# Kernel optimization log

Hardware: AMD Instinct MI355X
Metric: run time of the kernel (lower is better)

## Reference

```python
import jax, jax.numpy as jnp
import numpy as np

NUM_USERS = 50000
NUM_ITEMS = 50000
N_NODES = NUM_USERS + NUM_ITEMS
NNZ = 3200000
EMB_DIM = 64
N_LAYERS = 3
BATCH = 16384


def setup_inputs() -> dict:
    key = jax.random.key(0)
    ks = jax.random.split(key, 7)
    user_emb = 0.1 * jax.random.normal(ks[0], (NUM_USERS, EMB_DIM), dtype=jnp.float32)
    item_emb = 0.1 * jax.random.normal(ks[1], (NUM_ITEMS, EMB_DIM), dtype=jnp.float32)
    edge_val = jax.random.uniform(ks[2], (NNZ,), dtype=jnp.float32)
    edge_src = jax.random.randint(ks[3], (NNZ,), 0, N_NODES, dtype=jnp.int32)
    edge_dst = jax.random.randint(ks[4], (NNZ,), 0, N_NODES, dtype=jnp.int32)
    users = jax.random.randint(ks[5], (BATCH,), 0, NUM_USERS, dtype=jnp.int32)
    items = jax.random.randint(ks[6], (BATCH,), 0, NUM_ITEMS, dtype=jnp.int32)
    return {"user_emb": user_emb, "item_emb": item_emb, "edge_val": edge_val,
            "edge_src": edge_src, "edge_dst": edge_dst, "users": users, "items": items}


def _computer(user_emb, item_emb, edge_val, edge_src, edge_dst):
    # LightGCN propagation: all_emb <- A @ all_emb, mean over layer outputs (incl. layer 0)
    all_emb = jnp.concatenate([user_emb, item_emb], axis=0)  # [N, D]
    acc = all_emb
    for _ in range(N_LAYERS):
        msg = edge_val[:, None] * all_emb[edge_src]          # [nnz, D]
        all_emb = jax.ops.segment_sum(msg, edge_dst, num_segments=N_NODES)
        acc = acc + all_emb
    light_out = acc / jnp.float32(N_LAYERS + 1)
    return light_out[:NUM_USERS], light_out[NUM_USERS:]


def reference(user_emb, item_emb, edge_val, edge_src, edge_dst, users, items):
    all_users, all_items = _computer(user_emb, item_emb, edge_val, edge_src, edge_dst)
    users_emb = all_users[users]                              # [B, D]
    items_emb = all_items[items]                              # [B, D]
    gamma = jnp.sum(users_emb * items_emb, axis=1)            # [B]
    return gamma
```

## Files before the change

### kernel.cpp

```cpp
#include <hip/hip_runtime.h>

#define NUM_USERS 50000
#define NUM_ITEMS 50000
#define N_NODES   100000
#define NNZ       3200000
#define EMB_DIM   64
#define N_LAYERS  3
#define BATCH     16384

#define NBUCK 512
#define ABITS 8
#define NODES_PER_BUCK 256
#define TILE_EDGES 8192
#define NBUCK_USED ((N_NODES + NODES_PER_BUCK - 1) / NODES_PER_BUCK)
#define CAP 9216

typedef unsigned long long ull;

__device__ inline unsigned bf16pair(float a, float b) {
    unsigned ua = __float_as_uint(a), ub = __float_as_uint(b);
    unsigned r0 = (ua + 0x7fffu + ((ua >> 16) & 1u)) >> 16;
    unsigned r1 = (ub + 0x7fffu + ((ub >> 16) & 1u)) >> 16;
    return r0 | (r1 << 16);
}

__device__ inline void acc8(float* s, uint4 g, float w) {
    s[0] = fmaf(w, __uint_as_float(g.x << 16),        s[0]);
    s[1] = fmaf(w, __uint_as_float(g.x & 0xffff0000u), s[1]);
    s[2] = fmaf(w, __uint_as_float(g.y << 16),        s[2]);
    s[3] = fmaf(w, __uint_as_float(g.y & 0xffff0000u), s[3]);
    s[4] = fmaf(w, __uint_as_float(g.z << 16),        s[4]);
    s[5] = fmaf(w, __uint_as_float(g.z & 0xffff0000u), s[5]);
    s[6] = fmaf(w, __uint_as_float(g.w << 16),        s[6]);
    s[7] = fmaf(w, __uint_as_float(g.w & 0xffff0000u), s[7]);
}

__global__ void init_emb_kernel(const float* __restrict__ ue,
                                const float* __restrict__ ie,
                                unsigned* __restrict__ bufA16,
                                float* __restrict__ acc,
                                int* __restrict__ bucketCursor) {
    int idx = blockIdx.x * blockDim.x + threadIdx.x;
    if (blockIdx.x == 0 && threadIdx.x < 256) {
        bucketCursor[threadIdx.x]       = threadIdx.x * CAP;
        bucketCursor[threadIdx.x + 256] = (threadIdx.x + 256) * CAP;
    }
    const int total = N_NODES * (EMB_DIM / 4);
    if (idx >= total) return;
    const int uoff = NUM_USERS * (EMB_DIM / 4);
    float4 v;
    if (idx < uoff) v = ((const float4*)ue)[idx];
    else            v = ((const float4*)ie)[idx - uoff];
    ((float4*)acc)[idx] = v;
    uint2 h;
    h.x = bf16pair(v.x, v.y);
    h.y = bf16pair(v.z, v.w);
    ((uint2*)bufA16)[idx] = h;
}

__global__ void partA_kernel(const float* __restrict__ ev,
                             const int*  __restrict__ es,
                             const int*  __restrict__ ed,
                             int* __restrict__ bucketCursor,
                             ull* __restrict__ tmp) {
    __shared__ int hist[NBUCK];
    __shared__ int base[NBUCK];
    __shared__ int cnt2[NBUCK];
    int tid = threadIdx.x;
    int e0 = blockIdx.x * TILE_EDGES;

    int      mySrc[8], myDst[8];
    unsigned myQ[8];

    for (int i = tid; i < NBUCK; i += 1024) hist[i] = 0;
    __syncthreads();

    #pragma unroll
    for (int k = 0; k < 8; ++k) {
        int e = e0 + k * 1024 + tid;
        if (e < NNZ) {
            mySrc[k] = es[e];
            myDst[k] = ed[e];
            myQ[k]   = (unsigned)fminf(ev[e] * 32768.f + 0.5f, 32767.f);
            atomicAdd(&hist[((unsigned)myDst[k]) >> ABITS], 1);
        } else {
            myDst[k] = -1;
        }
    }
    __syncthreads();

    for (int i = tid; i < NBUCK; i += 1024) {
        int c = hist[i];
        base[i] = c ? atomicAdd(&bucketCursor[i], c) : 0;
        cnt2[i] = 0;
    }
    __syncthreads();

    #pragma unroll
    for (int k = 0; k < 8; ++k) {
        int dst = myDst[k];
        if (dst < 0) continue;
        int b = ((unsigned)dst) >> ABITS;
        int pos = base[b] + atomicAdd(&cnt2[b], 1);
        if (pos < (b + 1) * CAP) {
            ull rec = (ull)(unsigned)(mySrc[k] | ((dst & (NODES_PER_BUCK - 1)) << 17))
                    | ((ull)myQ[k] << 25);
            tmp[pos] = rec;
        }
    }
}

__global__ void partB_kernel(const ull* __restrict__ tmp,
                             const int* __restrict__ bucketCursor,
                             int* __restrict__ rowStart,
                             int* __restrict__ deg,
                             unsigned* __restrict__ sorted) {
    __shared__ int cnt[NODES_PER_BUCK];
    __shared__ int sc[NODES_PER_BUCK];
    __shared__ int cur[NODES_PER_BUCK];
    int b = blockIdx.x;
    int tid = threadIdx.x;
    int nodeLo = b << ABITS;
    int startE = b * CAP;
    int endE   = bucketCursor[b];

    if (tid < NODES_PER_BUCK) cnt[tid] = 0;
    __syncthreads();
    for (int i = startE + tid; i < endE; i += 1024) {
        ull rec = tmp[i];
        atomicAdd(&cnt[(int)((rec >> 17) & (NODES_PER_BUCK - 1))], 1);
    }
    __syncthreads();
    if (tid < NODES_PER_BUCK) sc[tid] = cnt[tid];
    __syncthreads();
    for (int o = 1; o < NODES_PER_BUCK; o <<= 1) {
        int add = 0;
        if (tid < NODES_PER_BUCK && tid >= o) add = sc[tid - o];
        __syncthreads();
        if (tid < NODES_PER_BUCK) sc[tid] += add;
        __syncthreads();
    }
    if (tid < NODES_PER_BUCK) {
        int node = nodeLo + tid;
        int rs = startE + sc[tid] - cnt[tid];
        cur[tid] = rs;
        if (node < N_NODES) {
            rowStart[node] = rs;
            deg[node] = cnt[tid];
        }
    }
    __syncthreads();
    for (int i = startE + tid; i < endE; i += 1024) {
        ull rec = tmp[i];
        int dl = (int)((rec >> 17) & (NODES_PER_BUCK - 1));
        unsigned o = (unsigned)(rec & 0x1FFFFULL) | ((unsigned)((rec >> 25) & 0x7FFF) << 17);
        int pos = atomicAdd(&cur[dl], 1);
        sorted[pos] = o;
    }
}

__global__ void pull_kernel(const uint4* __restrict__ A16,
                            uint4* __restrict__ B16,
                            float* __restrict__ acc,
                            const unsigned* __restrict__ sorted,
                            const int* __restrict__ rowStart,
                            const int* __restrict__ deg,
                            int writeB) {
    int t = blockIdx.x * blockDim.x + threadIdx.x;
    int node = t >> 6;
    if (node >= N_NODES) return;
    int lane = t & 63;
    int eg = lane >> 3;
    int d8 = lane & 7;
    int start = rowStart[node];
    int cnt   = deg[node];
    const unsigned* ep = sorted + start;
    const float k15 = 1.f / 32768.f;

    float s[8] = {0.f,0.f,0.f,0.f,0.f,0.f,0.f,0.f};
    int j = 0;
    while (j + 32 <= cnt) {
        unsigned r0 = ep[j + eg], r1 = ep[j + 8 + eg];
        unsigned r2 = ep[j + 16 + eg], r3 = ep[j + 24 + eg];
        uint4 g0 = A16[(((long long)(r0 & 0x1FFFFu)) << 3) + d8];
        uint4 g1 = A16[(((long long)(r1 & 0x1FFFFu)) << 3) + d8];
        uint4 g2 = A16[(((long long)(r2 & 0x1FFFFu)) << 3) + d8];
        uint4 g3 = A16[(((long long)(r3 & 0x1FFFFu)) << 3) + d8];
        acc8(s, g0, (float)(r0 >> 17) * k15);
        acc8(s, g1, (float)(r1 >> 17) * k15);
        acc8(s, g2, (float)(r2 >> 17) * k15);
        acc8(s, g3, (float)(r3 >> 17) * k15);
        j += 32;
    }
    while (j + 16 <= cnt) {
        unsigned r0 = ep[j + eg], r1 = ep[j + 8 + eg];
        uint4 g0 = A16[(((long long)(r0 & 0x1FFFFu)) << 3) + d8];
        uint4 g1 = A16[(((long long)(r1 & 0x1FFFFu)) << 3) + d8];
        acc8(s, g0, (float)(r0 >> 17) * k15);
        acc8(s, g1, (float)(r1 >> 17) * k15);
        j += 16;
    }
    for (; j < cnt; j += 8) {
        int idx = j + eg;
        unsigned r = (idx < cnt) ? ep[idx] : 0u;
        uint4 g = A16[(((long long)(r & 0x1FFFFu)) << 3) + d8];
        acc8(s, g, (float)(r >> 17) * k15);
    }
    #pragma unroll
    for (int k = 0; k < 8; ++k) {
        s[k] += __shfl_xor(s[k], 8, 64);
        s[k] += __shfl_xor(s[k], 16, 64);
        s[k] += __shfl_xor(s[k], 32, 64);
    }
    if (eg == 0) {
        float4* C4 = (float4*)acc;
        long long o = ((long long)node << 4) + d8 * 2;
        float4 c0 = C4[o], c1 = C4[o + 1];
        c0.x += s[0]; c0.y += s[1]; c0.z += s[2]; c0.w += s[3];
        c1.x += s[4]; c1.y += s[5]; c1.z += s[6]; c1.w += s[7];
        C4[o] = c0; C4[o + 1] = c1;
        if (writeB) {
            uint4 h;
            h.x = bf16pair(s[0], s[1]);
            h.y = bf16pair(s[2], s[3]);
            h.z = bf16pair(s[4], s[5]);
            h.w = bf16pair(s[6], s[7]);
            B16[(((long long)node) << 3) + d8] = h;
        }
    }
}

__global__ void dot_kernel(const float* __restrict__ acc,
                           const int* __restrict__ users,
                           const int* __restrict__ items,
                           float* __restrict__ out) {
    int t = blockIdx.x * blockDim.x + threadIdx.x;
    int b = t >> 6;
    int d = t & 63;
    if (b >= BATCH) return;
    int u  = users[b];
    int it = items[b] + NUM_USERS;
    float p = acc[(long long)u * EMB_DIM + d] * acc[(long long)it * EMB_DIM + d];
    #pragma unroll
    for (int off = 32; off >= 1; off >>= 1)
        p += __shfl_down(p, off, 64);
    if (d == 0) out[b] = p * 0.0625f;
}

extern "C" void kernel_launch(void* const* d_in, const int* in_sizes, int n_in,
                              void* d_out, int out_size, void* d_ws, size_t ws_size,
                              hipStream_t stream) {
    const float* user_emb = (const float*)d_in[0];
    const float* item_emb = (const float*)d_in[1];
    const float* edge_val = (const float*)d_in[2];
    const int*   edge_src = (const int*)d_in[3];
    const int*   edge_dst = (const int*)d_in[4];
    const int*   users    = (const int*)d_in[5];
    const int*   items    = (const int*)d_in[6];
    float* out = (float*)d_out;

    const size_t emb16Bytes = (size_t)N_NODES * EMB_DIM * 2;
    const size_t embBytes   = (size_t)N_NODES * EMB_DIM * sizeof(float);
    const size_t sortBytes  = (size_t)NBUCK_USED * CAP * sizeof(unsigned);
    const size_t tmpBytes   = (size_t)NBUCK_USED * CAP * sizeof(ull);
    const size_t nodeBytes  = (size_t)N_NODES * sizeof(int);

    char* w = (char*)d_ws;
    unsigned* bufA16       = (unsigned*)(w); w += emb16Bytes;
    unsigned* bufB16       = (unsigned*)(w); w += emb16Bytes;
    float*    acc          = (float*)(w);    w += embBytes;
    unsigned* sorted       = (unsigned*)(w); w += sortBytes;
    ull*      tmp          = (ull*)(w);      w += tmpBytes;
    int*      deg          = (int*)(w);      w += nodeBytes;
    int*      rowStart     = (int*)(w);      w += nodeBytes;
    int*      bucketCursor = (int*)(w);      w += NBUCK * sizeof(int);

    const int vecTotal   = N_NODES * (EMB_DIM / 4);
    const int initBlocks = (vecTotal + 255) / 256;
    const int tileBlocks = (NNZ + TILE_EDGES - 1) / TILE_EDGES;

    init_emb_kernel<<<initBlocks, 256, 0, stream>>>(user_emb, item_emb,
                                                    bufA16, acc, bucketCursor);

    partA_kernel<<<tileBlocks, 1024, 0, stream>>>(edge_val, edge_src, edge_dst,
                                                  bucketCursor, tmp);
    partB_kernel<<<NBUCK_USED, 1024, 0, stream>>>(tmp, bucketCursor,
                                                  rowStart, deg, sorted);

    const int pullBlocks = (N_NODES * 64 + 255) / 256;
    for (int layer = 0; layer < N_LAYERS; ++layer) {
        pull_kernel<<<pullBlocks, 256, 0, stream>>>((const uint4*)bufA16, (uint4*)bufB16,
                                                    acc, sorted, rowStart, deg,
                                                    layer < N_LAYERS - 1 ? 1 : 0);
        unsigned* tswap = bufA16; bufA16 = bufB16; bufB16 = tswap;
    }

    const int dotBlocks = (BATCH * 64 + 255) / 256;
    dot_kernel<<<dotBlocks, 256, 0, stream>>>(acc, users, items, out);
}
```

Baseline: 334.8 us.

## Skip last-layer propagation for nodes not referenced by the batch

Marks nodes used by the user/item batch in a bitmap and restricts the final propagation layer to those nodes, since only their accumulated embeddings feed the output. Also keeps bucket records in registers in the partition kernel instead of re-reading them from global memory. Adds a small flagging kernel with atomics and leaves acc incomplete for unqueried nodes.

```diff
diff --git a/kernel.cpp b/kernel.cpp
--- a/kernel.cpp
+++ b/kernel.cpp
@@ -14,6 +14,7 @@
 #define TILE_EDGES 8192
 #define NBUCK_USED ((N_NODES + NODES_PER_BUCK - 1) / NODES_PER_BUCK)
 #define CAP 9216
+#define BM_WORDS ((N_NODES + 31) / 32)
 
 typedef unsigned long long ull;
 
@@ -39,11 +40,15 @@
                                 const float* __restrict__ ie,
                                 unsigned* __restrict__ bufA16,
                                 float* __restrict__ acc,
-                                int* __restrict__ bucketCursor) {
+                                int* __restrict__ bucketCursor,
+                                unsigned* __restrict__ bitmap) {
     int idx = blockIdx.x * blockDim.x + threadIdx.x;
-    if (blockIdx.x == 0 && threadIdx.x < 256) {
-        bucketCursor[threadIdx.x]       = threadIdx.x * CAP;
-        bucketCursor[threadIdx.x + 256] = (threadIdx.x + 256) * CAP;
+    if (blockIdx.x == 0) {
+        if (threadIdx.x < 256) {
+            bucketCursor[threadIdx.x]       = threadIdx.x * CAP;
+            bucketCursor[threadIdx.x + 256] = (threadIdx.x + 256) * CAP;
+        }
+        for (int i = threadIdx.x; i < BM_WORDS; i += 256) bitmap[i] = 0;
     }
     const int total = N_NODES * (EMB_DIM / 4);
     if (idx >= total) return;
@@ -56,6 +61,19 @@
     h.x = bf16pair(v.x, v.y);
     h.y = bf16pair(v.z, v.w);
     ((uint2*)bufA16)[idx] = h;
+}
+
+__global__ void flag_kernel(const int* __restrict__ users,
+                            const int* __restrict__ items,
+                            unsigned* __restrict__ bitmap) {
+    int t = blockIdx.x * blockDim.x + threadIdx.x;
+    if (t < BATCH) {
+        int n = users[t];
+        atomicOr(&bitmap[n >> 5], 1u << (n & 31));
+    } else if (t < 2 * BATCH) {
+        int n = NUM_USERS + items[t - BATCH];
+        atomicOr(&bitmap[n >> 5], 1u << (n & 31));
+    }
 }
 
 __global__ void partA_kernel(const float* __restrict__ ev,
@@ -126,11 +144,20 @@
 
     if (tid < NODES_PER_BUCK) cnt[tid] = 0;
     __syncthreads();
-    for (int i = startE + tid; i < endE; i += 1024) {
-        ull rec = tmp[i];
-        atomicAdd(&cnt[(int)((rec >> 17) & (NODES_PER_BUCK - 1))], 1);
-    }
-    __syncthreads();
+
+    ull myRec[9];
+    int nRec = 0;
+    #pragma unroll
+    for (int k = 0; k < 9; ++k) {
+        int i = startE + k * 1024 + tid;
+        if (i < endE) {
+            myRec[k] = tmp[i];
+            nRec = k + 1;
+            atomicAdd(&cnt[(int)((myRec[k] >> 17) & (NODES_PER_BUCK - 1))], 1);
+        }
+    }
+    __syncthreads();
+
     if (tid < NODES_PER_BUCK) sc[tid] = cnt[tid];
     __syncthreads();
     for (int o = 1; o < NODES_PER_BUCK; o <<= 1) {
@@ -150,8 +177,9 @@
         }
     }
     __syncthreads();
-    for (int i = startE + tid; i < endE; i += 1024) {
-        ull rec = tmp[i];
+
+    for (int k = 0; k < nRec; ++k) {
+        ull rec = myRec[k];
         int dl = (int)((rec >> 17) & (NODES_PER_BUCK - 1));
         unsigned o = (unsigned)(rec & 0x1FFFFULL) | ((unsigned)((rec >> 25) & 0x7FFF) << 17);
         int pos = atomicAdd(&cur[dl], 1);
@@ -165,10 +193,12 @@
                             const unsigned* __restrict__ sorted,
                             const int* __restrict__ rowStart,
                             const int* __restrict__ deg,
-                            int writeB) {
+                            const unsigned* __restrict__ bitmap,
+                            int writeB, int gate) {
     int t = blockIdx.x * blockDim.x + threadIdx.x;
     int node = t >> 6;
     if (node >= N_NODES) return;
+    if (gate && !((bitmap[node >> 5] >> (node & 31)) & 1u)) return;
     int lane = t & 63;
     int eg = lane >> 3;
     int d8 = lane & 7;
@@ -274,13 +304,15 @@
     int*      deg          = (int*)(w);      w += nodeBytes;
     int*      rowStart     = (int*)(w);      w += nodeBytes;
     int*      bucketCursor = (int*)(w);      w += NBUCK * sizeof(int);
+    unsigned* bitmap       = (unsigned*)(w); w += BM_WORDS * sizeof(unsigned);
 
     const int vecTotal   = N_NODES * (EMB_DIM / 4);
     const int initBlocks = (vecTotal + 255) / 256;
     const int tileBlocks = (NNZ + TILE_EDGES - 1) / TILE_EDGES;
 
     init_emb_kernel<<<initBlocks, 256, 0, stream>>>(user_emb, item_emb,
-                                                    bufA16, acc, bucketCursor);
+                                                    bufA16, acc, bucketCursor, bitmap);
+    flag_kernel<<<(2 * BATCH + 255) / 256, 256, 0, stream>>>(users, items, bitmap);
 
     partA_kernel<<<tileBlocks, 1024, 0, stream>>>(edge_val, edge_src, edge_dst,
                                                   bucketCursor, tmp);
@@ -289,9 +321,10 @@
 
     const int pullBlocks = (N_NODES * 64 + 255) / 256;
     for (int layer = 0; layer < N_LAYERS; ++layer) {
+        int last = (layer == N_LAYERS - 1);
         pull_kernel<<<pullBlocks, 256, 0, stream>>>((const uint4*)bufA16, (uint4*)bufB16,
-                                                    acc, sorted, rowStart, deg,
-                                                    layer < N_LAYERS - 1 ? 1 : 0);
+                                                    acc, sorted, rowStart, deg, bitmap,
+                                                    last ? 0 : 1, last ? 1 : 0);
         unsigned* tswap = bufA16; bufA16 = bufB16; bufB16 = tswap;
     }
 
```

Measured after the change: 307.9 us. -8.0%, faster.
